# Kernel tuning notes

Measured on AMD Instinct MI355X. Metric: run time of the kernel, lower is better.

## Reference

```python
import jax, jax.numpy as jnp
import numpy as np

B, S, D = 4, 2048, 1024


def setup_inputs() -> dict:
    key = jax.random.key(0)
    k1, k2, k3 = jax.random.split(key, 3)
    x = jax.random.normal(k1, (B, S, D), dtype=jnp.float32)
    # torch nn.Linear weights are [out_features, in_features]
    wq_w = jax.random.normal(k2, (D, D), dtype=jnp.float32) * (1.0 / np.sqrt(D))
    wv_w = jax.random.normal(k3, (D, D), dtype=jnp.float32) * (1.0 / np.sqrt(D))
    return {"x": x, "wq_w": wq_w, "wv_w": wv_w}


def reference(x, wq_w, wv_w):
    b, s, d = x.shape
    q = x @ wq_w.T                      # [B,S,D]
    kv = x @ wv_w.T                     # [B,S,D]  (original uses wv for BOTH k and v; wk unused)
    # original: k.view(B, k_dim, -1) -- a raw memory RESHAPE, not a transpose
    k_r = kv.reshape(b, d, s)           # [B,D,S]
    scores = jnp.einsum('bsd,bdt->bst', q, k_r) / np.sqrt(d)  # [B,S,S]
    sm = jax.nn.softmax(scores, axis=-1)
    sm = jnp.tril(sm)                   # post-softmax causal mask (rows NOT renormalized)
    return jnp.einsum('bst,btd->bsd', sm, kv)
```

## Files before the change

### kernel.cpp

```cpp
#include <hip/hip_runtime.h>


typedef __attribute__((ext_vector_type(8))) _Float16 f16x8;
typedef __attribute__((ext_vector_type(4))) _Float16 f16x4;
typedef __attribute__((ext_vector_type(4))) float f32x4;

__device__ __forceinline__ void glds16(const void* g, void* l) {
  __builtin_amdgcn_global_load_lds((const __attribute__((address_space(1))) void*)g,
                                   (__attribute__((address_space(3))) void*)l, 16, 0, 0);
}
#define BAR() __builtin_amdgcn_s_barrier()
#define LGKM0() do { asm volatile("s_waitcnt lgkmcnt(0)" ::: "memory"); \
                     __builtin_amdgcn_sched_barrier(0); } while (0)
#define VM2() asm volatile("s_waitcnt vmcnt(2)" ::: "memory")
#define VM0() asm volatile("s_waitcnt vmcnt(0)" ::: "memory")
#define PR1() __builtin_amdgcn_s_setprio(1)
#define PR0() __builtin_amdgcn_s_setprio(0)

__global__ __launch_bounds__(256) void cvt3(const float* __restrict__ x,
                                            const float* __restrict__ wq,
                                            const float* __restrict__ wv,
                                            _Float16* __restrict__ xh,
                                            _Float16* __restrict__ wqh,
                                            _Float16* __restrict__ wvh) {
  int i = blockIdx.x * 256 + threadIdx.x;
  const float* src;
  _Float16* dst;
  int off;
  if (i < 2097152) { src = x; dst = xh; off = i; }
  else if (i < 2359296) { src = wq; dst = wqh; off = i - 2097152; }
  else { src = wv; dst = wvh; off = i - 2359296; }
  float4 v = ((const float4*)src)[off];
  f16x4 o = {(_Float16)v.x, (_Float16)v.y, (_Float16)v.z, (_Float16)v.w};
  ((f16x4*)dst)[off] = o;
}

__global__ __launch_bounds__(256) void transpose_f16(const _Float16* __restrict__ in,
                                                     _Float16* __restrict__ out,
                                                     int R, int C) {
  __shared__ _Float16 T[64][65];
  const size_t off = (size_t)blockIdx.z * R * C;
  const _Float16* I = in + off;
  _Float16* O = out + off;
  const int c0 = blockIdx.x * 64, r0 = blockIdx.y * 64;
  const int t = threadIdx.x;
#pragma unroll
  for (int i = 0; i < 2; ++i) {
    int lin = (t + i * 256) * 8;
    int r = lin >> 6, c = lin & 63;
    uint4 v = *(const uint4*)(I + (size_t)(r0 + r) * C + c0 + c);
    const _Float16* h = (const _Float16*)&v;
#pragma unroll
    for (int j = 0; j < 8; ++j) T[r][c + j] = h[j];
  }
  __syncthreads();
#pragma unroll
  for (int i = 0; i < 2; ++i) {
    int lin = (t + i * 256) * 8;
    int cc = lin >> 6, rr = lin & 63;
    _Float16 o[8];
#pragma unroll
    for (int j = 0; j < 8; ++j) o[j] = T[rr + j][cc];
    *(uint4*)(O + (size_t)(c0 + cc) * R + r0 + rr) = *(const uint4*)o;
  }
}

template <typename OUT_T>
__global__ __launch_bounds__(512, 2) void gemm8p(const _Float16* __restrict__ A,
                                                 const _Float16* __restrict__ BT,
                                                 OUT_T* __restrict__ C,
                                                 int K, int ldc,
                                                 long sA, long sB, long sC, float scale,
                                                 int lgx, int lgy) {
  extern __shared__ char smem[];
  _Float16* lds = (_Float16*)smem;
  {
    int lin = blockIdx.x + gridDim.x * (blockIdx.y + gridDim.y * blockIdx.z);
    const int xcd = lin & 7, s = lin >> 3;
    const int G = (gridDim.y * gridDim.z) >> 3;
    const int mx = s & ((1 << lgx) - 1);
    const int pid = xcd * G + (s >> lgx);
    const int ny = pid & (gridDim.y - 1);
    const int bz = pid >> lgy;
    A += (size_t)bz * sA;
    BT += (size_t)bz * sB;
    C += (size_t)bz * sC;
    lin = 0;
    A += (size_t)0;
    __builtin_amdgcn_sched_barrier(0);
    static_assert(true, "");
    goto after_remap;
  after_remap:;
    const int m0_ = mx << 8, n0_ = ny << 8;
    const int tid = threadIdx.x, lane = tid & 63, wave = tid >> 6;
    const int wm = wave >> 2, wn = wave & 3;
    const int lr = lane & 15, lk = lane >> 4, xr = lane & 7;
    const int nkt = K >> 6;
    const int A0 = 0, A1 = 8192, B0 = 16384, B1 = 24576, BUF = 32768;
    const int baseA = wm ? A1 : A0;
    const int baseB = B0 + ((wn >> 1) << 13);
    const int bRow = (wn & 1) << 6;
    const int srow = lane >> 3;
    const int scolB = ((lane & 7) << 4) ^ (srow << 4);
    const int m0 = m0_, n0 = n0_;

    f32x4 acc[8][4] = {};
    f16x8 fa[4][2], fb[4][2];

#define STAGE(bufsel, halfsel, G_, hrow0, kt) do {                                   \
    const _Float16* _g = (G_) + (size_t)((hrow0) + wave * 16 + srow) * K + ((kt) << 6); \
    glds16((const char*)_g + scolB, (char*)&lds[(bufsel) * BUF + (halfsel) + wave * 1024]); \
    glds16((const char*)(_g + (size_t)8 * K) + scolB,                                \
           (char*)&lds[(bufsel) * BUF + (halfsel) + wave * 1024 + 512]);             \
  } while (0)
#define RDA(buf, mf, ks) (*(const f16x8*)&lds[(buf) * BUF + baseA + ((mf) * 16 + lr) * 64 + \
                                              ((((ks) * 4 + lk) ^ xr) << 3)])
#define RDB(buf, nf, ks) (*(const f16x8*)&lds[(buf) * BUF + baseB + (bRow + (nf) * 16 + lr) * 64 + \
                                              ((((ks) * 4 + lk) ^ xr) << 3)])
#define RDFA4(b, mbase) do { _Pragma("unroll")                                        \
    for (int i = 0; i < 4; ++i) { fa[i][0] = RDA(b, (mbase) + i, 0);                  \
                                  fa[i][1] = RDA(b, (mbase) + i, 1); } } while (0)
#define RDFB2(b, jbase) do { _Pragma("unroll")                                        \
    for (int j = 0; j < 2; ++j) { fb[(jbase) + j][0] = RDB(b, (jbase) + j, 0);        \
                                  fb[(jbase) + j][1] = RDB(b, (jbase) + j, 1); } } while (0)
#define MMQ(ib, jb) do { _Pragma("unroll")                                            \
    for (int i = 0; i < 4; ++i) { _Pragma("unroll")                                   \
      for (int j = 0; j < 2; ++j) {                                                   \
        acc[(ib) + i][(jb) + j] = __builtin_amdgcn_mfma_f32_16x16x32_f16(             \
            fa[i][0], fb[(jb) + j][0], acc[(ib) + i][(jb) + j], 0, 0, 0);             \
        acc[(ib) + i][(jb) + j] = __builtin_amdgcn_mfma_f32_16x16x32_f16(             \
            fa[i][1], fb[(jb) + j][1], acc[(ib) + i][(jb) + j], 0, 0, 0);             \
      } } } while (0)

    STAGE(0, A0, A, m0, 0);
    STAGE(0, A1, A, m0 + 128, 0);
    STAGE(0, B0, BT, n0, 0);
    STAGE(0, B1, BT, n0 + 128, 0);
    STAGE(1, A0, A, m0, 1);
    VM2();
    BAR();

    for (int it = 0; it < (nkt >> 1); ++it) {
      const int t = it << 1;
      const int t2 = (t + 2 < nkt) ? t + 2 : 0;
      const int t3 = (t + 3 < nkt) ? t + 3 : 0;
      RDFA4(0, 0); RDFB2(0, 0);
      STAGE(1, A1, A, m0 + 128, t + 1);
      STAGE(1, B0, BT, n0, t + 1);
      BAR(); LGKM0(); PR1(); MMQ(0, 0); PR0(); BAR();
      RDFB2(0, 2);
      STAGE(1, B1, BT, n0 + 128, t + 1);
      BAR(); LGKM0(); PR1(); MMQ(0, 2); PR0(); BAR();
      RDFA4(0, 4);
      BAR(); LGKM0(); PR1(); MMQ(4, 2); PR0(); BAR();
      STAGE(0, A0, A, m0, t2);
      VM2();
      BAR(); PR1(); MMQ(4, 0); PR0(); BAR();
      RDFA4(1, 0); RDFB2(1, 0);
      STAGE(0, A1, A, m0 + 128, t2);
      STAGE(0, B0, BT, n0, t2);
      BAR(); LGKM0(); PR1(); MMQ(0, 0); PR0(); BAR();
      RDFB2(1, 2);
      STAGE(0, B1, BT, n0 + 128, t2);
      BAR(); LGKM0(); PR1(); MMQ(0, 2); PR0(); BAR();
      RDFA4(1, 4);
      BAR(); LGKM0(); PR1(); MMQ(4, 2); PR0(); BAR();
      STAGE(1, A0, A, m0, t3);
      VM2();
      BAR(); PR1(); MMQ(4, 0); PR0(); BAR();
    }

#pragma unroll
    for (int mf = 0; mf < 8; ++mf)
#pragma unroll
      for (int nf = 0; nf < 4; ++nf) {
        const int row = m0 + wm * 128 + mf * 16 + lk * 4;
        const int col = n0 + wn * 64 + nf * 16 + lr;
#pragma unroll
        for (int r = 0; r < 4; ++r)
          C[(size_t)(row + r) * ldc + col] = (OUT_T)(acc[mf][nf][r] * scale);
      }
#undef STAGE
#undef RDA
#undef RDB
#undef RDFA4
#undef RDFB2
#undef MMQ
  }
}

__global__ __launch_bounds__(256) void gemm_pv_bal(const _Float16* __restrict__ P,
                                                   const _Float16* __restrict__ KVT,
                                                   float* __restrict__ Out,
                                                   long sA, long sB, long sC) {
  __shared__ _Float16 As[2][64 * 64];
  __shared__ _Float16 Bs[2][128 * 64];
  const int total = gridDim.x * gridDim.y * gridDim.z;
  int lin = blockIdx.x + gridDim.x * (blockIdx.y + gridDim.y * blockIdx.z);
  const int xcd = lin & 7, slot = lin >> 3;
  const int perx = total >> 7;
  const int grp = xcd * perx + (slot >> 4);
  const int p = slot & 15;
  const int ny = grp & 7, bz = grp >> 3;
  P += (size_t)bz * sA;
  KVT += (size_t)bz * sB;
  Out += (size_t)bz * sC;
  const int n0 = ny * 128;
  const int lane = threadIdx.x & 63, wave = threadIdx.x >> 6;
  const int fr = lane & 15, lk = lane >> 4;
  const int srow = lane >> 3;
  const int scol = (((lane & 7) ^ srow) << 4);

#define PSTAGE(buf, m0s, t) do {                                                     \
    const int _k0 = (t) << 6;                                                        \
    _Pragma("unroll")                                                                \
    for (int c = 0; c < 2; ++c) {                                                    \
      const int ch = wave * 2 + c;                                                   \
      glds16((const char*)(P + (size_t)((m0s) + ch * 8 + srow) * 2048 + _k0) + scol, \
             &As[buf][ch * 512]);                                                    \
    }                                                                                \
    _Pragma("unroll")                                                                \
    for (int c = 0; c < 4; ++c) {                                                    \
      const int ch = wave * 4 + c;                                                   \
      glds16((const char*)(KVT + (size_t)(n0 + ch * 8 + srow) * 2048 + _k0) + scol,  \
             &Bs[buf][ch * 512]);                                                    \
    }                                                                                \
  } while (0)

#pragma unroll
  for (int half = 0; half < 2; ++half) {
    const int strip = half ? (31 - p) : p;
    const int m0s = strip * 64;
    const int nt = strip + 1;
    f32x4 acc[4][2] = {};
    PSTAGE(0, m0s, 0);
    VM0();
    BAR();
    for (int t = 0; t < nt; ++t) {
      const int cur = t & 1;
      if (t + 1 < nt) PSTAGE(cur ^ 1, m0s, t + 1);
      f16x8 af[4][2], bf[2][2];
#pragma unroll
      for (int m = 0; m < 4; ++m) {
        const int r = m * 16 + fr;
#pragma unroll
        for (int ks = 0; ks < 2; ++ks)
          af[m][ks] = *(const f16x8*)&As[cur][r * 64 + (((ks * 4 + lk) ^ (r & 7)) << 3)];
      }
#pragma unroll
      for (int n = 0; n < 2; ++n) {
        const int rb = wave * 32 + n * 16 + fr;
#pragma unroll
        for (int ks = 0; ks < 2; ++ks)
          bf[n][ks] = *(const f16x8*)&Bs[cur][rb * 64 + (((ks * 4 + lk) ^ (rb & 7)) << 3)];
      }
      LGKM0();
      PR1();
#pragma unroll
      for (int ks = 0; ks < 2; ++ks)
#pragma unroll
        for (int m = 0; m < 4; ++m)
#pragma unroll
          for (int n = 0; n < 2; ++n)
            acc[m][n] = __builtin_amdgcn_mfma_f32_16x16x32_f16(af[m][ks], bf[n][ks],
                                                               acc[m][n], 0, 0, 0);
      PR0();
      VM0();
      BAR();
    }
#pragma unroll
    for (int m = 0; m < 4; ++m)
#pragma unroll
      for (int n = 0; n < 2; ++n) {
        const int row = m0s + m * 16 + lk * 4;
        const int col = n0 + wave * 32 + n * 16 + fr;
#pragma unroll
        for (int r = 0; r < 4; ++r)
          Out[(size_t)(row + r) * 1024 + col] = acc[m][n][r];
      }
  }
#undef PSTAGE
}

__global__ __launch_bounds__(256) void softmax_mask(_Float16* __restrict__ S) {
  const int row = blockIdx.x;
  const int s = row & 2047;
  _Float16* p = S + (size_t)row * 2048;
  const int tid = threadIdx.x;
  uint4 u = ((const uint4*)p)[tid];
  const _Float16* h = (const _Float16*)&u;
  float v[8];
#pragma unroll
  for (int j = 0; j < 8; ++j) v[j] = (float)h[j];
  float mx = v[0];
#pragma unroll
  for (int j = 1; j < 8; ++j) mx = fmaxf(mx, v[j]);
#pragma unroll
  for (int off = 32; off > 0; off >>= 1) mx = fmaxf(mx, __shfl_xor(mx, off));
  __shared__ float red[8];
  const int wave = tid >> 6, lane = tid & 63;
  if (lane == 0) red[wave] = mx;
  __syncthreads();
  mx = fmaxf(fmaxf(red[0], red[1]), fmaxf(red[2], red[3]));
  float se = 0.f;
#pragma unroll
  for (int j = 0; j < 8; ++j) se += __expf(v[j] - mx);
#pragma unroll
  for (int off = 32; off > 0; off >>= 1) se += __shfl_xor(se, off);
  if (lane == 0) red[4 + wave] = se;
  __syncthreads();
  const float inv = 1.f / (red[4] + red[5] + red[6] + red[7]);
  const int lim = (s & ~63) + 64;
  if (tid * 8 < lim) {
    _Float16 o[8];
#pragma unroll
    for (int j = 0; j < 8; ++j) {
      int t = tid * 8 + j;
      o[j] = (_Float16)((t <= s) ? __expf(v[j] - mx) * inv : 0.f);
    }
    ((uint4*)p)[tid] = *(const uint4*)o;
  }
}

extern "C" void kernel_launch(void* const* d_in, const int* in_sizes, int n_in,
                              void* d_out, int out_size, void* d_ws, size_t ws_size,
                              hipStream_t stream) {
  const float* x = (const float*)d_in[0];
  const float* wq = (const float*)d_in[1];
  const float* wv = (const float*)d_in[2];
  float* out = (float*)d_out;
  char* ws = (char*)d_ws;

  const size_t MB = 1024 * 1024;
  const int bc = (ws_size >= 96 * MB) ? 4 : 2;
  const size_t scBytes = (size_t)bc * 2048 * 2048 * 2;
  const long PB = 2048 * 1024;
  const long SB = (long)2048 * 2048;

  _Float16* Sc = (_Float16*)ws;
  _Float16* qh = (_Float16*)(ws + scBytes);
  _Float16* kvh = (_Float16*)(ws + scBytes + 16 * MB);
  _Float16* kvvT = (_Float16*)(ws + scBytes + 32 * MB);
  _Float16* kvT = (_Float16*)(ws + scBytes + 48 * MB);
  _Float16* xh = (_Float16*)ws;
  _Float16* wqh = (_Float16*)(ws + 16 * MB);
  _Float16* wvh = (_Float16*)(ws + 18 * MB);

  cvt3<<<10240, 256, 0, stream>>>(x, wq, wv, xh, wqh, wvh);

  gemm8p<_Float16><<<dim3(32, 4, 2), 512, 131072, stream>>>(
      xh, wqh, qh, 1024, 1024, 0, (long)(wvh - wqh), (long)(kvh - qh), 1.0f, 5, 2);

  transpose_f16<<<dim3(32, 16, 4), 256, 0, stream>>>(kvh, kvvT, 1024, 2048);
  transpose_f16<<<dim3(16, 32, 4), 256, 0, stream>>>(kvh, kvT, 2048, 1024);

  for (int b0 = 0; b0 < 4; b0 += bc) {
    gemm8p<_Float16><<<dim3(8, 8, bc), 512, 131072, stream>>>(
        qh + (size_t)b0 * PB, kvvT + (size_t)b0 * PB, Sc,
        1024, 2048, PB, PB, SB, 0.03125f, 3, 3);
    softmax_mask<<<bc * 2048, 256, 0, stream>>>(Sc);
    gemm_pv_bal<<<dim3(16, 8, bc), 256, 0, stream>>>(
        Sc, kvT + (size_t)b0 * PB, out + (size_t)b0 * PB, SB, PB, PB);
  }
}
```

Before: 144.4 us.

## Fuse KV transposes into projection GEMM epilogue and shrink workspace

The projection GEMM now writes the KV result directly in both transposed layouts (kvT and the reshaped kvvT) from its accumulators, which removes the two separate transpose kernels and the kvh intermediate buffer. The workspace layout is repacked so that all four batches fit under a lower threshold (85 MB), letting the attention loop run in a single pass more often. The epilogue uses narrow strided stores (4- and 8-byte) scattered across rows, which may coalesce poorly compared with the row-major store path.

After: 166.3 us. 1.15x slower.

```diff
diff --git a/kernel.cpp b/kernel.cpp
--- a/kernel.cpp
+++ b/kernel.cpp
@@ -16,6 +16,12 @@
 #define VM0() asm volatile("s_waitcnt vmcnt(0)" ::: "memory")
 #define PR1() __builtin_amdgcn_s_setprio(1)
 #define PR0() __builtin_amdgcn_s_setprio(0)
+
+__device__ __forceinline__ unsigned pkh2(float a, float b) {
+  union { _Float16 h[2]; unsigned u; } c;
+  c.h[0] = (_Float16)a; c.h[1] = (_Float16)b;
+  return c.u;
+}
 
 __global__ __launch_bounds__(256) void cvt3(const float* __restrict__ x,
                                             const float* __restrict__ wq,
@@ -35,77 +41,41 @@
   ((f16x4*)dst)[off] = o;
 }
 
-__global__ __launch_bounds__(256) void transpose_f16(const _Float16* __restrict__ in,
-                                                     _Float16* __restrict__ out,
-                                                     int R, int C) {
-  __shared__ _Float16 T[64][65];
-  const size_t off = (size_t)blockIdx.z * R * C;
-  const _Float16* I = in + off;
-  _Float16* O = out + off;
-  const int c0 = blockIdx.x * 64, r0 = blockIdx.y * 64;
-  const int t = threadIdx.x;
-#pragma unroll
-  for (int i = 0; i < 2; ++i) {
-    int lin = (t + i * 256) * 8;
-    int r = lin >> 6, c = lin & 63;
-    uint4 v = *(const uint4*)(I + (size_t)(r0 + r) * C + c0 + c);
-    const _Float16* h = (const _Float16*)&v;
-#pragma unroll
-    for (int j = 0; j < 8; ++j) T[r][c + j] = h[j];
-  }
-  __syncthreads();
-#pragma unroll
-  for (int i = 0; i < 2; ++i) {
-    int lin = (t + i * 256) * 8;
-    int cc = lin >> 6, rr = lin & 63;
-    _Float16 o[8];
-#pragma unroll
-    for (int j = 0; j < 8; ++j) o[j] = T[rr + j][cc];
-    *(uint4*)(O + (size_t)(c0 + cc) * R + r0 + rr) = *(const uint4*)o;
-  }
-}
-
-template <typename OUT_T>
+template <typename OUT_T, int EPI>
 __global__ __launch_bounds__(512, 2) void gemm8p(const _Float16* __restrict__ A,
                                                  const _Float16* __restrict__ BT,
                                                  OUT_T* __restrict__ C,
+                                                 _Float16* __restrict__ T1,
+                                                 _Float16* __restrict__ T2,
                                                  int K, int ldc,
                                                  long sA, long sB, long sC, float scale,
                                                  int lgx, int lgy) {
   extern __shared__ char smem[];
   _Float16* lds = (_Float16*)smem;
-  {
-    int lin = blockIdx.x + gridDim.x * (blockIdx.y + gridDim.y * blockIdx.z);
-    const int xcd = lin & 7, s = lin >> 3;
-    const int G = (gridDim.y * gridDim.z) >> 3;
-    const int mx = s & ((1 << lgx) - 1);
-    const int pid = xcd * G + (s >> lgx);
-    const int ny = pid & (gridDim.y - 1);
-    const int bz = pid >> lgy;
-    A += (size_t)bz * sA;
-    BT += (size_t)bz * sB;
-    C += (size_t)bz * sC;
-    lin = 0;
-    A += (size_t)0;
-    __builtin_amdgcn_sched_barrier(0);
-    static_assert(true, "");
-    goto after_remap;
-  after_remap:;
-    const int m0_ = mx << 8, n0_ = ny << 8;
-    const int tid = threadIdx.x, lane = tid & 63, wave = tid >> 6;
-    const int wm = wave >> 2, wn = wave & 3;
-    const int lr = lane & 15, lk = lane >> 4, xr = lane & 7;
-    const int nkt = K >> 6;
-    const int A0 = 0, A1 = 8192, B0 = 16384, B1 = 24576, BUF = 32768;
-    const int baseA = wm ? A1 : A0;
-    const int baseB = B0 + ((wn >> 1) << 13);
-    const int bRow = (wn & 1) << 6;
-    const int srow = lane >> 3;
-    const int scolB = ((lane & 7) << 4) ^ (srow << 4);
-    const int m0 = m0_, n0 = n0_;
-
-    f32x4 acc[8][4] = {};
-    f16x8 fa[4][2], fb[4][2];
+  const int lin = blockIdx.x + gridDim.x * (blockIdx.y + gridDim.y * blockIdx.z);
+  const int xcd = lin & 7, s = lin >> 3;
+  const int G = (gridDim.y * gridDim.z) >> 3;
+  const int mx = s & ((1 << lgx) - 1);
+  const int pid = xcd * G + (s >> lgx);
+  const int ny = pid & (gridDim.y - 1);
+  const int bz = pid >> lgy;
+  A += (size_t)bz * sA;
+  BT += (size_t)bz * sB;
+  C += (size_t)bz * sC;
+  const int m0 = mx << 8, n0 = ny << 8;
+  const int tid = threadIdx.x, lane = tid & 63, wave = tid >> 6;
+  const int wm = wave >> 2, wn = wave & 3;
+  const int lr = lane & 15, lk = lane >> 4, xr = lane & 7;
+  const int nkt = K >> 6;
+  const int A0 = 0, A1 = 8192, B0 = 16384, B1 = 24576, BUF = 32768;
+  const int baseA = wm ? A1 : A0;
+  const int baseB = B0 + ((wn >> 1) << 13);
+  const int bRow = (wn & 1) << 6;
+  const int srow = lane >> 3;
+  const int scolB = ((lane & 7) << 4) ^ (srow << 4);
+
+  f32x4 acc[8][4] = {};
+  f16x8 fa[4][2], fb[4][2];
 
 #define STAGE(bufsel, halfsel, G_, hrow0, kt) do {                                   \
     const _Float16* _g = (G_) + (size_t)((hrow0) + wave * 16 + srow) * K + ((kt) << 6); \
@@ -132,44 +102,64 @@
             fa[i][1], fb[(jb) + j][1], acc[(ib) + i][(jb) + j], 0, 0, 0);             \
       } } } while (0)
 
-    STAGE(0, A0, A, m0, 0);
-    STAGE(0, A1, A, m0 + 128, 0);
-    STAGE(0, B0, BT, n0, 0);
-    STAGE(0, B1, BT, n0 + 128, 0);
-    STAGE(1, A0, A, m0, 1);
+  STAGE(0, A0, A, m0, 0);
+  STAGE(0, A1, A, m0 + 128, 0);
+  STAGE(0, B0, BT, n0, 0);
+  STAGE(0, B1, BT, n0 + 128, 0);
+  STAGE(1, A0, A, m0, 1);
+  VM2();
+  BAR();
+
+  for (int it = 0; it < (nkt >> 1); ++it) {
+    const int t = it << 1;
+    const int t2 = (t + 2 < nkt) ? t + 2 : 0;
+    const int t3 = (t + 3 < nkt) ? t + 3 : 0;
+    RDFA4(0, 0); RDFB2(0, 0);
+    STAGE(1, A1, A, m0 + 128, t + 1);
+    STAGE(1, B0, BT, n0, t + 1);
+    BAR(); LGKM0(); PR1(); MMQ(0, 0); PR0(); BAR();
+    RDFB2(0, 2);
+    STAGE(1, B1, BT, n0 + 128, t + 1);
+    BAR(); LGKM0(); PR1(); MMQ(0, 2); PR0(); BAR();
+    RDFA4(0, 4);
+    BAR(); LGKM0(); PR1(); MMQ(4, 2); PR0(); BAR();
+    STAGE(0, A0, A, m0, t2);
     VM2();
-    BAR();
-
-    for (int it = 0; it < (nkt >> 1); ++it) {
-      const int t = it << 1;
-      const int t2 = (t + 2 < nkt) ? t + 2 : 0;
-      const int t3 = (t + 3 < nkt) ? t + 3 : 0;
-      RDFA4(0, 0); RDFB2(0, 0);
-      STAGE(1, A1, A, m0 + 128, t + 1);
-      STAGE(1, B0, BT, n0, t + 1);
-      BAR(); LGKM0(); PR1(); MMQ(0, 0); PR0(); BAR();
-      RDFB2(0, 2);
-      STAGE(1, B1, BT, n0 + 128, t + 1);
-      BAR(); LGKM0(); PR1(); MMQ(0, 2); PR0(); BAR();
-      RDFA4(0, 4);
-      BAR(); LGKM0(); PR1(); MMQ(4, 2); PR0(); BAR();
-      STAGE(0, A0, A, m0, t2);
-      VM2();
-      BAR(); PR1(); MMQ(4, 0); PR0(); BAR();
-      RDFA4(1, 0); RDFB2(1, 0);
-      STAGE(0, A1, A, m0 + 128, t2);
-      STAGE(0, B0, BT, n0, t2);
-      BAR(); LGKM0(); PR1(); MMQ(0, 0); PR0(); BAR();
-      RDFB2(1, 2);
-      STAGE(0, B1, BT, n0 + 128, t2);
-      BAR(); LGKM0(); PR1(); MMQ(0, 2); PR0(); BAR();
-      RDFA4(1, 4);
-      BAR(); LGKM0(); PR1(); MMQ(4, 2); PR0(); BAR();
-      STAGE(1, A0, A, m0, t3);
-      VM2();
-      BAR(); PR1(); MMQ(4, 0); PR0(); BAR();
-    }
-
+    BAR(); PR1(); MMQ(4, 0); PR0(); BAR();
+    RDFA4(1, 0); RDFB2(1, 0);
+    STAGE(0, A1, A, m0 + 128, t2);
+    STAGE(0, B0, BT, n0, t2);
+    BAR(); LGKM0(); PR1(); MMQ(0, 0); PR0(); BAR();
+    RDFB2(1, 2);
+    STAGE(0, B1, BT, n0 + 128, t2);
+    BAR(); LGKM0(); PR1(); MMQ(0, 2); PR0(); BAR();
+    RDFA4(1, 4);
+    BAR(); LGKM0(); PR1(); MMQ(4, 2); PR0(); BAR();
+    STAGE(1, A0, A, m0, t3);
+    VM2();
+    BAR(); PR1(); MMQ(4, 0); PR0(); BAR();
+  }
+
+  if (EPI == 1 && bz == 1) {
+    const int b = m0 >> 11;
+    _Float16* kvvT = T1 + ((size_t)b << 21);
+    _Float16* kvT  = T2 + ((size_t)b << 21);
+    const int tb = m0 & 2047;
+#pragma unroll
+    for (int mf = 0; mf < 8; ++mf)
+#pragma unroll
+      for (int nf = 0; nf < 4; ++nf) {
+        const int t0 = tb + wm * 128 + mf * 16 + lk * 4;
+        const int d = n0 + wn * 64 + nf * 16 + lr;
+        const f32x4 a = acc[mf][nf];
+        unsigned lo = pkh2(a[0], a[1]), hi = pkh2(a[2], a[3]);
+        uint2 w8 = {lo, hi};
+        *(uint2*)(kvT + (size_t)d * 2048 + t0) = w8;
+        const int k0 = t0 >> 1;
+        *(unsigned*)(kvvT + (size_t)d * 1024 + k0) = pkh2(a[0], a[2]);
+        *(unsigned*)(kvvT + (size_t)(1024 + d) * 1024 + k0) = pkh2(a[1], a[3]);
+      }
+  } else {
 #pragma unroll
     for (int mf = 0; mf < 8; ++mf)
 #pragma unroll
@@ -180,13 +170,13 @@
         for (int r = 0; r < 4; ++r)
           C[(size_t)(row + r) * ldc + col] = (OUT_T)(acc[mf][nf][r] * scale);
       }
+  }
 #undef STAGE
 #undef RDA
 #undef RDB
 #undef RDFA4
 #undef RDFB2
 #undef MMQ
-  }
 }
 
 __global__ __launch_bounds__(256) void gemm_pv_bal(const _Float16* __restrict__ P,
@@ -332,31 +322,27 @@
   char* ws = (char*)d_ws;
 
   const size_t MB = 1024 * 1024;
-  const int bc = (ws_size >= 96 * MB) ? 4 : 2;
+  const int bc = (ws_size >= 85 * MB) ? 4 : 2;
   const size_t scBytes = (size_t)bc * 2048 * 2048 * 2;
   const long PB = 2048 * 1024;
   const long SB = (long)2048 * 2048;
 
   _Float16* Sc = (_Float16*)ws;
   _Float16* qh = (_Float16*)(ws + scBytes);
-  _Float16* kvh = (_Float16*)(ws + scBytes + 16 * MB);
-  _Float16* kvvT = (_Float16*)(ws + scBytes + 32 * MB);
-  _Float16* kvT = (_Float16*)(ws + scBytes + 48 * MB);
+  _Float16* kvvT = (_Float16*)(ws + scBytes + 16 * MB);
+  _Float16* kvT = (_Float16*)(ws + scBytes + 32 * MB);
+  _Float16* wqh = (_Float16*)(ws + scBytes + 48 * MB);
+  _Float16* wvh = (_Float16*)(ws + scBytes + 50 * MB);
   _Float16* xh = (_Float16*)ws;
-  _Float16* wqh = (_Float16*)(ws + 16 * MB);
-  _Float16* wvh = (_Float16*)(ws + 18 * MB);
 
   cvt3<<<10240, 256, 0, stream>>>(x, wq, wv, xh, wqh, wvh);
 
-  gemm8p<_Float16><<<dim3(32, 4, 2), 512, 131072, stream>>>(
-      xh, wqh, qh, 1024, 1024, 0, (long)(wvh - wqh), (long)(kvh - qh), 1.0f, 5, 2);
-
-  transpose_f16<<<dim3(32, 16, 4), 256, 0, stream>>>(kvh, kvvT, 1024, 2048);
-  transpose_f16<<<dim3(16, 32, 4), 256, 0, stream>>>(kvh, kvT, 2048, 1024);
+  gemm8p<_Float16, 1><<<dim3(32, 4, 2), 512, 131072, stream>>>(
+      xh, wqh, qh, kvvT, kvT, 1024, 1024, 0, (long)(wvh - wqh), 0, 1.0f, 5, 2);
 
   for (int b0 = 0; b0 < 4; b0 += bc) {
-    gemm8p<_Float16><<<dim3(8, 8, bc), 512, 131072, stream>>>(
-        qh + (size_t)b0 * PB, kvvT + (size_t)b0 * PB, Sc,
+    gemm8p<_Float16, 0><<<dim3(8, 8, bc), 512, 131072, stream>>>(
+        qh + (size_t)b0 * PB, kvvT + (size_t)b0 * PB, Sc, nullptr, nullptr,
         1024, 2048, PB, PB, SB, 0.03125f, 3, 3);
     softmax_mask<<<bc * 2048, 256, 0, stream>>>(Sc);
     gemm_pv_bal<<<dim3(16, 8, bc), 256, 0, stream>>>(
```
